# Optimization experiments

Hardware: AMD Instinct MI355X
Metric: run time of the kernel (lower is better)

Reference implementation:

```python
import jax, jax.numpy as jnp
import numpy as np

EPS = 1e-06


def _conv1x1(x, W, b):
    # x: [B,C,H,W], W: [O,C], b: [O] -> [B,O,H,W]
    return jnp.einsum('oc,bchw->bohw', W, x) + b[None, :, None, None]


def _l2_norm(x):
    # normalize over channel dim (-2) per position, matching torch.norm(p=2, dim=-2)
    return x / jnp.linalg.norm(x, axis=-2, keepdims=True)


def setup_inputs() -> dict:
    key = jax.random.key(0)
    ks = jax.random.split(key, 8)
    B, C, H, W = 8, 512, 64, 64
    Cq = C // 8
    s = 0.02
    return {
        'x': jax.random.normal(ks[0], (B, C, H, W), jnp.float32),
        'Wq': jax.random.normal(ks[1], (Cq, C), jnp.float32) * s,
        'bq': jax.random.normal(ks[2], (Cq,), jnp.float32) * s,
        'Wk': jax.random.normal(ks[3], (Cq, C), jnp.float32) * s,
        'bk': jax.random.normal(ks[4], (Cq,), jnp.float32) * s,
        'Wv': jax.random.normal(ks[5], (C, C), jnp.float32) * s,
        'bv': jax.random.normal(ks[6], (C,), jnp.float32) * s,
        'gamma': jax.random.normal(ks[7], (1,), jnp.float32),
    }


def reference(x, Wq, bq, Wk, bk, Wv, bv, gamma):
    B, C, H, W = x.shape
    N = H * W
    Q = _conv1x1(x, Wq, bq).reshape(B, -1, N)   # [B,C',N]
    K = _conv1x1(x, Wk, bk).reshape(B, -1, N)   # [B,C',N]
    V = _conv1x1(x, Wv, bv).reshape(B, C, N)    # [B,C,N]

    Qn = _l2_norm(Q).transpose(0, 2, 1)         # [B,N,C']
    Kn = _l2_norm(K)                            # [B,C',N]

    # taylor denominator: 1 / (N + Q . (sum_n K + eps))
    tailor_sum = 1.0 / (N + jnp.einsum('bnc,bc->bn', Qn, Kn.sum(-1) + EPS))  # [B,N]

    value_sum = V.sum(-1)                        # [B,C]
    matrix = jnp.einsum('bmn,bcn->bmc', Kn, V)   # [B,C',C]
    matrix_sum = value_sum[:, :, None] + jnp.einsum('bnm,bmc->bcn', Qn, matrix)  # [B,C,N]

    weight_value = (matrix_sum * tailor_sum[:, None, :]).reshape(B, C, H, W)
    return gamma * weight_value
```

## Files before the change

### kernel.cpp

```cpp
#include <hip/hip_runtime.h>
#include <math.h>

#define B_   8
#define C_   512
#define CQ   64
#define N_   4096
#define EPSF 1e-6f
#define LS   40
#define LS2  72

typedef short  shortx8 __attribute__((ext_vector_type(8)));
typedef short  shortx4 __attribute__((ext_vector_type(4)));
typedef short  shortx2 __attribute__((ext_vector_type(2)));
typedef float  floatx4 __attribute__((ext_vector_type(4)));
typedef float  floatx2 __attribute__((ext_vector_type(2)));

__device__ __forceinline__ short f2bf(float f) {
    unsigned u = __builtin_bit_cast(unsigned, f);
    u += 0x7FFFu + ((u >> 16) & 1u);
    return (short)(u >> 16);
}
__device__ __forceinline__ float bf2f(short h) {
    unsigned u = ((unsigned)(unsigned short)h) << 16;
    return __builtin_bit_cast(float, u);
}
__device__ __forceinline__ shortx8 ldf8(const short* p) {
    return *(const shortx8*)p;
}

__global__ __launch_bounds__(256) void pcast(
    const float* __restrict__ Wq, const float* __restrict__ Wk,
    const float* __restrict__ Wv, short* __restrict__ Wqk, short* __restrict__ Wvb)
{
    int i = (blockIdx.x * 256 + threadIdx.x) * 4;
    float4 v; short* dst;
    if (i < 2 * CQ * C_) {
        const float* src = (i < CQ * C_) ? (Wq + i) : (Wk + i - CQ * C_);
        v = *(const float4*)src;
        dst = Wqk + i;
    } else {
        int j = i - 2 * CQ * C_;
        v = *(const float4*)(Wv + j);
        dst = Wvb + j;
    }
    const float* f = (const float*)&v;
    shortx4 o = { f2bf(f[0]), f2bf(f[1]), f2bf(f[2]), f2bf(f[3]) };
    *(shortx4*)dst = o;
}

__global__ __launch_bounds__(256, 4) void k1_qk(
    const float* __restrict__ x, const short* __restrict__ Wqk,
    const float* __restrict__ bq, const float* __restrict__ bk,
    short* __restrict__ Qnt, short* __restrict__ Kn, float* __restrict__ Ksum)
{
    const int b   = blockIdx.y;
    const int n0  = blockIdx.x * 32;
    const int tid = threadIdx.x;
    const int lane = tid & 63, wid = tid >> 6;
    const int waveM = wid >> 1, waveN = wid & 1;
    const int quad = lane >> 4, ln = lane & 15;

    __shared__ short A_l[2][128][LS];
    __shared__ short B_l[2][32][LS];
    __shared__ float bias_l[128];

    if (tid < 128) bias_l[tid] = (tid < 64) ? bq[tid] : bk[tid - 64];

    const int mA = tid >> 1, koA = (tid & 1) * 16;
    const short* Asrc = Wqk + (size_t)mA * C_;
    const int kp = tid >> 4, nq = tid & 15;
    const float* xb = x + (size_t)b * C_ * N_;

    shortx8 a0 = *(const shortx8*)(Asrc + koA);
    shortx8 a1 = *(const shortx8*)(Asrc + koA + 8);
    floatx2 r0, r1;
    {
        const float* Bs = xb + (size_t)(kp * 2) * N_ + n0 + nq * 2;
        r0 = *(const floatx2*)(Bs);
        r1 = *(const floatx2*)(Bs + N_);
    }

    auto stage = [&](int buf, shortx8 s0, shortx8 s1, floatx2 q0, floatx2 q1) {
        *(shortx8*)&A_l[buf][mA][koA]     = s0;
        *(shortx8*)&A_l[buf][mA][koA + 8] = s1;
        shortx2 t0 = { f2bf(q0[0]), f2bf(q1[0]) };
        shortx2 t1 = { f2bf(q0[1]), f2bf(q1[1]) };
        *(shortx2*)&B_l[buf][nq * 2][kp * 2]     = t0;
        *(shortx2*)&B_l[buf][nq * 2 + 1][kp * 2] = t1;
    };
    stage(0, a0, a1, r0, r1);
    __syncthreads();

    const floatx4 z4 = {0.f, 0.f, 0.f, 0.f};
    floatx4 acc[4] = {z4, z4, z4, z4};

    int cur = 0;
    for (int it = 0; it < 16; ++it) {
        shortx8 na0, na1; floatx2 nr0, nr1;
        if (it < 15) {
            const int k0 = (it + 1) * 32;
            na0 = *(const shortx8*)(Asrc + k0 + koA);
            na1 = *(const shortx8*)(Asrc + k0 + koA + 8);
            const float* Bs = xb + (size_t)(k0 + kp * 2) * N_ + n0 + nq * 2;
            nr0 = *(const floatx2*)(Bs);
            nr1 = *(const floatx2*)(Bs + N_);
        }
        shortx8 af[4];
#pragma unroll
        for (int mt = 0; mt < 4; mt++)
            af[mt] = ldf8(&A_l[cur][waveM * 64 + mt * 16 + ln][quad * 8]);
        shortx8 bf8 = ldf8(&B_l[cur][waveN * 16 + ln][quad * 8]);
#pragma unroll
        for (int mt = 0; mt < 4; mt++)
            acc[mt] = __builtin_amdgcn_mfma_f32_16x16x32_bf16(af[mt], bf8, acc[mt], 0, 0, 0);
        if (it < 15) stage(cur ^ 1, na0, na1, nr0, nr1);
        __syncthreads();
        cur ^= 1;
    }

#pragma unroll
    for (int mt = 0; mt < 4; mt++)
#pragma unroll
        for (int r = 0; r < 4; r++)
            acc[mt][r] += bias_l[waveM * 64 + mt * 16 + quad * 4 + r];

    {
        float s = 0.f;
#pragma unroll
        for (int mt = 0; mt < 4; mt++)
#pragma unroll
            for (int r = 0; r < 4; r++) s += acc[mt][r] * acc[mt][r];
        s += __shfl_xor(s, 16);
        s += __shfl_xor(s, 32);
        float inv = rsqrtf(s);
#pragma unroll
        for (int mt = 0; mt < 4; mt++)
#pragma unroll
            for (int r = 0; r < 4; r++) acc[mt][r] *= inv;
    }

    const int n = n0 + waveN * 16 + ln;
    if (waveM == 0) {
        short* Qb = Qnt + (size_t)b * N_ * CQ;
#pragma unroll
        for (int mt = 0; mt < 4; mt++) {
            shortx4 v;
#pragma unroll
            for (int r = 0; r < 4; r++) v[r] = f2bf(acc[mt][r]);
            *(shortx4*)(Qb + (size_t)n * CQ + mt * 16 + quad * 4) = v;
        }
    } else {
        short* Kb = Kn + (size_t)b * CQ * N_;
#pragma unroll
        for (int mt = 0; mt < 4; mt++)
#pragma unroll
            for (int r = 0; r < 4; r++) {
                int m = mt * 16 + quad * 4 + r;
                float v = acc[mt][r];
                Kb[(size_t)m * N_ + n] = f2bf(v);
                float s = v;
                s += __shfl_xor(s, 1); s += __shfl_xor(s, 2);
                s += __shfl_xor(s, 4); s += __shfl_xor(s, 8);
                if (ln == 0) atomicAdd(&Ksum[b * CQ + m], s);
            }
    }
}

__global__ __launch_bounds__(256, 4) void k2_kx(
    const float* __restrict__ x, const short* __restrict__ Kn,
    float* __restrict__ KX, float* __restrict__ xsum)
{
    const int jt = blockIdx.x, ks = blockIdx.y, b = blockIdx.z;
    const int j0 = jt * 64, nbase = ks * 256;
    const int tid = threadIdx.x;
    const int lane = tid & 63, wid = tid >> 6;
    const int quad = lane >> 4, ln = lane & 15;

    __shared__ short A_l[2][64][LS];
    __shared__ short B_l[2][64][LS];

    const int rA = tid >> 2, oA = (tid & 3) * 8;
    const short* Kb = Kn + (size_t)b * CQ * N_;
    const float* xb = x + (size_t)b * C_ * N_;
    const short* As = Kb + (size_t)rA * N_ + nbase + oA;
    const float* Bs = xb + (size_t)(j0 + rA) * N_ + nbase + oA;

    float xsacc = 0.f;

    shortx8 aC = *(const shortx8*)As;
    float4 b0 = *(const float4*)(Bs);
    float4 b1 = *(const float4*)(Bs + 4);

    auto stage = [&](int buf, shortx8 a, float4 q0, float4 q1) {
        *(shortx8*)&A_l[buf][rA][oA] = a;
        const float* f0 = (const float*)&q0;
        const float* f1 = (const float*)&q1;
        shortx8 t;
#pragma unroll
        for (int i = 0; i < 4; i++) {
            t[i]     = f2bf(f0[i]); xsacc += f0[i];
            t[i + 4] = f2bf(f1[i]); xsacc += f1[i];
        }
        *(shortx8*)&B_l[buf][rA][oA] = t;
    };
    stage(0, aC, b0, b1);
    __syncthreads();

    const floatx4 z4 = {0.f, 0.f, 0.f, 0.f};
    floatx4 acc[4] = {z4, z4, z4, z4};

    int cur = 0;
    for (int it = 0; it < 8; ++it) {
        shortx8 aN; float4 n0v, n1v;
        if (it < 7) {
            const int off = (it + 1) * 32;
            aN  = *(const shortx8*)(As + off);
            n0v = *(const float4*)(Bs + off);
            n1v = *(const float4*)(Bs + off + 4);
        }
        shortx8 af[4];
#pragma unroll
        for (int mt = 0; mt < 4; mt++)
            af[mt] = ldf8(&A_l[cur][mt * 16 + ln][quad * 8]);
        shortx8 bf8 = ldf8(&B_l[cur][wid * 16 + ln][quad * 8]);
#pragma unroll
        for (int mt = 0; mt < 4; mt++)
            acc[mt] = __builtin_amdgcn_mfma_f32_16x16x32_bf16(af[mt], bf8, acc[mt], 0, 0, 0);
        if (it < 7) stage(cur ^ 1, aN, n0v, n1v);
        __syncthreads();
        cur ^= 1;
    }

    xsacc += __shfl_xor(xsacc, 1);
    xsacc += __shfl_xor(xsacc, 2);
    if ((tid & 3) == 0) atomicAdd(&xsum[b * C_ + j0 + rA], xsacc);

    float* KXb = KX + (size_t)b * CQ * C_;
#pragma unroll
    for (int mt = 0; mt < 4; mt++)
#pragma unroll
        for (int r = 0; r < 4; r++) {
            int m = mt * 16 + quad * 4 + r;
            atomicAdd(&KXb[(size_t)m * C_ + j0 + wid * 16 + ln], acc[mt][r]);
        }
}

__global__ __launch_bounds__(256, 2) void k3_m(
    const float* __restrict__ KX, const short* __restrict__ Wvb,
    const float* __restrict__ bv, const float* __restrict__ Ksum,
    const float* __restrict__ xsum,
    short* __restrict__ Mt, float* __restrict__ vs)
{
    const int ct = blockIdx.x, b = blockIdx.y;
    const int c0 = ct * 64;
    const int tid = threadIdx.x;
    const int lane = tid & 63, wid = tid >> 6;
    const int quad = lane >> 4, ln = lane & 15;

    __shared__ short A_l[2][64][LS];
    __shared__ short B_l[2][64][LS];
    __shared__ float xsl[C_], Ksl[64], bvl[64], vsp[4][64];

    xsl[tid] = xsum[(size_t)b * C_ + tid];
    xsl[tid + 256] = xsum[(size_t)b * C_ + tid + 256];
    if (tid < 64) { Ksl[tid] = Ksum[b * CQ + tid]; bvl[tid] = bv[c0 + tid]; }

    const int rA = tid >> 2, oA = (tid & 3) * 8;
    const short* As = Wvb + (size_t)(c0 + rA) * C_ + oA;
    const float* Bs = KX + ((size_t)b * CQ + rA) * C_ + oA;

    shortx8 aC = *(const shortx8*)As;
    float4 b0 = *(const float4*)(Bs);
    float4 b1 = *(const float4*)(Bs + 4);

    auto stage = [&](int buf, shortx8 a, float4 q0, float4 q1) {
        *(shortx8*)&A_l[buf][rA][oA] = a;
        const float* f0 = (const float*)&q0;
        const float* f1 = (const float*)&q1;
        shortx8 t;
#pragma unroll
        for (int i = 0; i < 4; i++) { t[i] = f2bf(f0[i]); t[i + 4] = f2bf(f1[i]); }
        *(shortx8*)&B_l[buf][rA][oA] = t;
    };
    stage(0, aC, b0, b1);
    __syncthreads();

    const floatx4 z4 = {0.f, 0.f, 0.f, 0.f};
    floatx4 acc[4] = {z4, z4, z4, z4};
    float vsacc = 0.f;
    const int cv = tid & 63;

    int cur = 0;
    for (int it = 0; it < 16; ++it) {
        shortx8 aN; float4 n0v, n1v;
        if (it < 15) {
            const int off = (it + 1) * 32;
            aN  = *(const shortx8*)(As + off);
            n0v = *(const float4*)(Bs + off);
            n1v = *(const float4*)(Bs + off + 4);
        }
        shortx8 af[4];
#pragma unroll
        for (int ct2 = 0; ct2 < 4; ct2++)
            af[ct2] = ldf8(&A_l[cur][ct2 * 16 + ln][quad * 8]);
        shortx8 bf8 = ldf8(&B_l[cur][wid * 16 + ln][quad * 8]);
#pragma unroll
        for (int ct2 = 0; ct2 < 4; ct2++)
            acc[ct2] = __builtin_amdgcn_mfma_f32_16x16x32_bf16(af[ct2], bf8, acc[ct2], 0, 0, 0);
#pragma unroll
        for (int jj = 0; jj < 8; jj++)
            vsacc += bf2f(A_l[cur][cv][wid * 8 + jj]) * xsl[it * 32 + wid * 8 + jj];
        if (it < 15) stage(cur ^ 1, aN, n0v, n1v);
        __syncthreads();
        cur ^= 1;
    }

    vsp[wid][cv] = vsacc;
    __syncthreads();
    if (tid < 64)
        vs[(size_t)b * C_ + c0 + tid] =
            vsp[0][tid] + vsp[1][tid] + vsp[2][tid] + vsp[3][tid] + (float)N_ * bvl[tid];

    const int m = wid * 16 + ln;
    const float ksm = Ksl[m];
    short* Mb = Mt + (size_t)b * C_ * CQ;
#pragma unroll
    for (int ct2 = 0; ct2 < 4; ct2++)
#pragma unroll
        for (int r = 0; r < 4; r++) {
            int c = ct2 * 16 + quad * 4 + r;
            Mb[(size_t)(c0 + c) * CQ + m] = f2bf(acc[ct2][r] + ksm * bvl[c]);
        }
}

__global__ __launch_bounds__(256, 3) void k4_out(
    const short* __restrict__ Qnt, const short* __restrict__ Mt,
    const float* __restrict__ vs, const float* __restrict__ Ksum,
    const float* __restrict__ gamma, float* __restrict__ out)
{
    const int nt = blockIdx.x, ct = blockIdx.y, b = blockIdx.z;
    const int n0 = nt * 128, c0 = ct * 128;
    const int tid = threadIdx.x;
    const int lane = tid & 63, wid = tid >> 6;
    const int waveC = wid >> 1, waveN = wid & 1;
    const int quad = lane >> 4, ln = lane & 15;

    __shared__ short A_l[128][LS2];
    __shared__ short B_l[128][LS2];
    __shared__ float tsl[128], vsl[128], Ks_l[64];

    {
        int c = tid >> 1, h = tid & 1;
        const short* src = Mt + ((size_t)b * C_ + c0 + c) * CQ + h * 32;
#pragma unroll
        for (int q = 0; q < 4; q++)
            *(shortx8*)&A_l[c][h * 32 + q * 8] = *(const shortx8*)(src + q * 8);
    }
    {
        int n = tid >> 1, h = tid & 1;
        const short* src = Qnt + ((size_t)b * N_ + n0 + n) * CQ + h * 32;
#pragma unroll
        for (int q = 0; q < 4; q++)
            *(shortx8*)&B_l[n][h * 32 + q * 8] = *(const shortx8*)(src + q * 8);
    }
    if (tid < 64)  Ks_l[tid] = Ksum[b * CQ + tid];
    if (tid < 128) vsl[tid]  = vs[(size_t)b * C_ + c0 + tid];
    __syncthreads();

    if (tid < 128) {
        const short* row = B_l[tid];
        float s = 0.f;
#pragma unroll
        for (int m = 0; m < 64; m++) s += bf2f(row[m]) * (Ks_l[m] + EPSF);
        tsl[tid] = 1.f / ((float)N_ + s);
    }
    __syncthreads();

    const floatx4 z4 = {0.f, 0.f, 0.f, 0.f};
    floatx4 acc[4][4];
#pragma unroll
    for (int i = 0; i < 4; i++)
#pragma unroll
        for (int j = 0; j < 4; j++) acc[i][j] = z4;

#pragma unroll
    for (int kc = 0; kc < 2; kc++) {
        shortx8 af[4];
#pragma unroll
        for (int ct2 = 0; ct2 < 4; ct2++)
            af[ct2] = ldf8(&A_l[waveC * 64 + ct2 * 16 + ln][kc * 32 + quad * 8]);
#pragma unroll
        for (int nt2 = 0; nt2 < 4; nt2++) {
            shortx8 bf8 = ldf8(&B_l[waveN * 64 + nt2 * 16 + ln][kc * 32 + quad * 8]);
#pragma unroll
            for (int ct2 = 0; ct2 < 4; ct2++)
                acc[ct2][nt2] = __builtin_amdgcn_mfma_f32_16x16x32_bf16(af[ct2], bf8, acc[ct2][nt2], 0, 0, 0);
        }
    }

    const float g = gamma[0];
    float* ob = out + (size_t)b * C_ * N_;
#pragma unroll
    for (int ct2 = 0; ct2 < 4; ct2++)
#pragma unroll
        for (int r = 0; r < 4; r++) {
            int cl = waveC * 64 + ct2 * 16 + quad * 4 + r;
            float vc = vsl[cl];
#pragma unroll
            for (int nt2 = 0; nt2 < 4; nt2++) {
                int nl = waveN * 64 + nt2 * 16 + ln;
                ob[(size_t)(c0 + cl) * N_ + n0 + nl] = g * tsl[nl] * (vc + acc[ct2][nt2][r]);
            }
        }
}

extern "C" void kernel_launch(void* const* d_in, const int* in_sizes, int n_in,
                              void* d_out, int out_size, void* d_ws, size_t ws_size,
                              hipStream_t stream)
{
    (void)in_sizes; (void)n_in; (void)out_size; (void)ws_size;
    const float* x     = (const float*)d_in[0];
    const float* Wq    = (const float*)d_in[1];
    const float* bq    = (const float*)d_in[2];
    const float* Wk    = (const float*)d_in[3];
    const float* bk    = (const float*)d_in[4];
    const float* Wv    = (const float*)d_in[5];
    const float* bv    = (const float*)d_in[6];
    const float* gamma = (const float*)d_in[7];
    float* out = (float*)d_out;

    short* Qnt = (short*)d_ws;
    short* Kn  = Qnt + (size_t)B_ * N_ * CQ;
    float* Ksum = (float*)(Kn + (size_t)B_ * CQ * N_);
    float* xsum = Ksum + B_ * CQ;
    float* KX   = xsum + B_ * C_;
    short* Mt   = (short*)(KX + (size_t)B_ * CQ * C_);
    float* vs   = (float*)(Mt + (size_t)B_ * C_ * CQ);
    short* Wqk  = (short*)(vs + B_ * C_);
    short* Wvb  = Wqk + 2 * CQ * C_;

    size_t zbytes = (size_t)(B_ * CQ + B_ * C_ + B_ * CQ * C_) * 4;
    hipMemsetAsync(Ksum, 0, zbytes, stream);

    pcast <<<dim3(320),       256, 0, stream>>>(Wq, Wk, Wv, Wqk, Wvb);
    k1_qk <<<dim3(128, 8),    256, 0, stream>>>(x, Wqk, bq, bk, Qnt, Kn, Ksum);
    k2_kx <<<dim3(8, 16, 8),  256, 0, stream>>>(x, Kn, KX, xsum);
    k3_m  <<<dim3(8, 8),      256, 0, stream>>>(KX, Wvb, bv, Ksum, xsum, Mt, vs);
    k4_out<<<dim3(32, 4, 8),  256, 0, stream>>>(Qnt, Mt, vs, Ksum, gamma, out);
}
```

Measured before the change: 214.4 us.

## Cast x to bf16 once in k1, reuse in k2; read MFMA operands directly from global

k1 now converts its whole 32-column slab of x to bf16 up front. It writes that bf16 copy to a workspace buffer and accumulates the per-channel x sums there, instead of pipelining fp32 x through double-buffered shared memory. k2 then reads the bf16 copy and Kn fragments straight from global memory, so it no longer re-reads fp32 x or computes xsum. k1 and k4 likewise load weight and Mt fragments directly from global instead of staging them in LDS. This halves the bytes of the second pass over x and removes the LDS staging and barriers. In exchange it adds an extra bf16 write of x, more atomics, and uncoalesced global fragment loads with no software prefetch.

New measurement: 259.3 us. +20.9%, slower.

```diff
diff --git a/kernel.cpp b/kernel.cpp
--- a/kernel.cpp
+++ b/kernel.cpp
@@ -8,12 +8,12 @@
 #define EPSF 1e-6f
 #define LS   40
 #define LS2  72
+#define LSK  520
 
 typedef short  shortx8 __attribute__((ext_vector_type(8)));
 typedef short  shortx4 __attribute__((ext_vector_type(4)));
 typedef short  shortx2 __attribute__((ext_vector_type(2)));
 typedef float  floatx4 __attribute__((ext_vector_type(4)));
-typedef float  floatx2 __attribute__((ext_vector_type(2)));
 
 __device__ __forceinline__ short f2bf(float f) {
     unsigned u = __builtin_bit_cast(unsigned, f);
@@ -51,7 +51,8 @@
 __global__ __launch_bounds__(256, 4) void k1_qk(
     const float* __restrict__ x, const short* __restrict__ Wqk,
     const float* __restrict__ bq, const float* __restrict__ bk,
-    short* __restrict__ Qnt, short* __restrict__ Kn, float* __restrict__ Ksum)
+    short* __restrict__ Qnt, short* __restrict__ Kn, short* __restrict__ xh,
+    float* __restrict__ Ksum, float* __restrict__ xsum)
 {
     const int b   = blockIdx.y;
     const int n0  = blockIdx.x * 32;
@@ -60,62 +61,50 @@
     const int waveM = wid >> 1, waveN = wid & 1;
     const int quad = lane >> 4, ln = lane & 15;
 
-    __shared__ short A_l[2][128][LS];
-    __shared__ short B_l[2][32][LS];
+    __shared__ __attribute__((aligned(16))) short B_l[32][LSK];
     __shared__ float bias_l[128];
 
     if (tid < 128) bias_l[tid] = (tid < 64) ? bq[tid] : bk[tid - 64];
 
-    const int mA = tid >> 1, koA = (tid & 1) * 16;
-    const short* Asrc = Wqk + (size_t)mA * C_;
-    const int kp = tid >> 4, nq = tid & 15;
-    const float* xb = x + (size_t)b * C_ * N_;
-
-    shortx8 a0 = *(const shortx8*)(Asrc + koA);
-    shortx8 a1 = *(const shortx8*)(Asrc + koA + 8);
-    floatx2 r0, r1;
-    {
-        const float* Bs = xb + (size_t)(kp * 2) * N_ + n0 + nq * 2;
-        r0 = *(const floatx2*)(Bs);
-        r1 = *(const floatx2*)(Bs + N_);
-    }
-
-    auto stage = [&](int buf, shortx8 s0, shortx8 s1, floatx2 q0, floatx2 q1) {
-        *(shortx8*)&A_l[buf][mA][koA]     = s0;
-        *(shortx8*)&A_l[buf][mA][koA + 8] = s1;
-        shortx2 t0 = { f2bf(q0[0]), f2bf(q1[0]) };
-        shortx2 t1 = { f2bf(q0[1]), f2bf(q1[1]) };
-        *(shortx2*)&B_l[buf][nq * 2][kp * 2]     = t0;
-        *(shortx2*)&B_l[buf][nq * 2 + 1][kp * 2] = t1;
-    };
-    stage(0, a0, a1, r0, r1);
-    __syncthreads();
-
+    const int k0 = tid * 2;
+    const float* xr0 = x  + (size_t)b * C_ * N_ + (size_t)k0 * N_ + n0;
+    short*       xh0 = xh + (size_t)b * C_ * N_ + (size_t)k0 * N_ + n0;
+    float xs0 = 0.f, xs1 = 0.f;
+#pragma unroll
+    for (int i = 0; i < 8; i++) {
+        float4 r0 = *(const float4*)(xr0 + i * 4);
+        float4 r1 = *(const float4*)(xr0 + N_ + i * 4);
+        const float* f0 = (const float*)&r0;
+        const float* f1 = (const float*)&r1;
+        shortx4 o0, o1;
+#pragma unroll
+        for (int j = 0; j < 4; j++) {
+            o0[j] = f2bf(f0[j]); xs0 += f0[j];
+            o1[j] = f2bf(f1[j]); xs1 += f1[j];
+            shortx2 t = { o0[j], o1[j] };
+            *(shortx2*)&B_l[i * 4 + j][k0] = t;
+        }
+        *(shortx4*)(xh0 + i * 4)      = o0;
+        *(shortx4*)(xh0 + N_ + i * 4) = o1;
+    }
+    atomicAdd(&xsum[b * C_ + k0],     xs0);
+    atomicAdd(&xsum[b * C_ + k0 + 1], xs1);
+    __syncthreads();
+
+    const short* Ab = Wqk + (size_t)(waveM * 64 + ln) * C_ + quad * 8;
     const floatx4 z4 = {0.f, 0.f, 0.f, 0.f};
     floatx4 acc[4] = {z4, z4, z4, z4};
 
-    int cur = 0;
-    for (int it = 0; it < 16; ++it) {
-        shortx8 na0, na1; floatx2 nr0, nr1;
-        if (it < 15) {
-            const int k0 = (it + 1) * 32;
-            na0 = *(const shortx8*)(Asrc + k0 + koA);
-            na1 = *(const shortx8*)(Asrc + k0 + koA + 8);
-            const float* Bs = xb + (size_t)(k0 + kp * 2) * N_ + n0 + nq * 2;
-            nr0 = *(const floatx2*)(Bs);
-            nr1 = *(const floatx2*)(Bs + N_);
-        }
+#pragma unroll 4
+    for (int kc = 0; kc < 16; ++kc) {
+        shortx8 bf8 = ldf8(&B_l[waveN * 16 + ln][kc * 32 + quad * 8]);
         shortx8 af[4];
 #pragma unroll
         for (int mt = 0; mt < 4; mt++)
-            af[mt] = ldf8(&A_l[cur][waveM * 64 + mt * 16 + ln][quad * 8]);
-        shortx8 bf8 = ldf8(&B_l[cur][waveN * 16 + ln][quad * 8]);
+            af[mt] = ldf8(Ab + (size_t)mt * 16 * C_ + kc * 32);
 #pragma unroll
         for (int mt = 0; mt < 4; mt++)
             acc[mt] = __builtin_amdgcn_mfma_f32_16x16x32_bf16(af[mt], bf8, acc[mt], 0, 0, 0);
-        if (it < 15) stage(cur ^ 1, na0, na1, nr0, nr1);
-        __syncthreads();
-        cur ^= 1;
     }
 
 #pragma unroll
@@ -167,8 +156,8 @@
 }
 
 __global__ __launch_bounds__(256, 4) void k2_kx(
-    const float* __restrict__ x, const short* __restrict__ Kn,
-    float* __restrict__ KX, float* __restrict__ xsum)
+    const short* __restrict__ xh, const short* __restrict__ Kn,
+    float* __restrict__ KX)
 {
     const int jt = blockIdx.x, ks = blockIdx.y, b = blockIdx.z;
     const int j0 = jt * 64, nbase = ks * 256;
@@ -176,64 +165,24 @@
     const int lane = tid & 63, wid = tid >> 6;
     const int quad = lane >> 4, ln = lane & 15;
 
-    __shared__ short A_l[2][64][LS];
-    __shared__ short B_l[2][64][LS];
-
-    const int rA = tid >> 2, oA = (tid & 3) * 8;
-    const short* Kb = Kn + (size_t)b * CQ * N_;
-    const float* xb = x + (size_t)b * C_ * N_;
-    const short* As = Kb + (size_t)rA * N_ + nbase + oA;
-    const float* Bs = xb + (size_t)(j0 + rA) * N_ + nbase + oA;
-
-    float xsacc = 0.f;
-
-    shortx8 aC = *(const shortx8*)As;
-    float4 b0 = *(const float4*)(Bs);
-    float4 b1 = *(const float4*)(Bs + 4);
-
-    auto stage = [&](int buf, shortx8 a, float4 q0, float4 q1) {
-        *(shortx8*)&A_l[buf][rA][oA] = a;
-        const float* f0 = (const float*)&q0;
-        const float* f1 = (const float*)&q1;
-        shortx8 t;
-#pragma unroll
-        for (int i = 0; i < 4; i++) {
-            t[i]     = f2bf(f0[i]); xsacc += f0[i];
-            t[i + 4] = f2bf(f1[i]); xsacc += f1[i];
-        }
-        *(shortx8*)&B_l[buf][rA][oA] = t;
-    };
-    stage(0, aC, b0, b1);
-    __syncthreads();
+    const short* Ab = Kn + (size_t)b * CQ * N_ + (size_t)ln * N_ + nbase + quad * 8;
+    const short* Bb = xh + (size_t)b * C_ * N_
+                    + (size_t)(j0 + wid * 16 + ln) * N_ + nbase + quad * 8;
 
     const floatx4 z4 = {0.f, 0.f, 0.f, 0.f};
     floatx4 acc[4] = {z4, z4, z4, z4};
 
-    int cur = 0;
-    for (int it = 0; it < 8; ++it) {
-        shortx8 aN; float4 n0v, n1v;
-        if (it < 7) {
-            const int off = (it + 1) * 32;
-            aN  = *(const shortx8*)(As + off);
-            n0v = *(const float4*)(Bs + off);
-            n1v = *(const float4*)(Bs + off + 4);
-        }
+#pragma unroll 4
+    for (int kc = 0; kc < 8; ++kc) {
+        shortx8 bf8 = ldf8(Bb + kc * 32);
         shortx8 af[4];
 #pragma unroll
         for (int mt = 0; mt < 4; mt++)
-            af[mt] = ldf8(&A_l[cur][mt * 16 + ln][quad * 8]);
-        shortx8 bf8 = ldf8(&B_l[cur][wid * 16 + ln][quad * 8]);
+            af[mt] = ldf8(Ab + (size_t)mt * 16 * N_ + kc * 32);
 #pragma unroll
         for (int mt = 0; mt < 4; mt++)
             acc[mt] = __builtin_amdgcn_mfma_f32_16x16x32_bf16(af[mt], bf8, acc[mt], 0, 0, 0);
-        if (it < 7) stage(cur ^ 1, aN, n0v, n1v);
-        __syncthreads();
-        cur ^= 1;
-    }
-
-    xsacc += __shfl_xor(xsacc, 1);
-    xsacc += __shfl_xor(xsacc, 2);
-    if ((tid & 3) == 0) atomicAdd(&xsum[b * C_ + j0 + rA], xsacc);
+    }
 
     float* KXb = KX + (size_t)b * CQ * C_;
 #pragma unroll
@@ -345,17 +294,9 @@
     const int waveC = wid >> 1, waveN = wid & 1;
     const int quad = lane >> 4, ln = lane & 15;
 
-    __shared__ short A_l[128][LS2];
     __shared__ short B_l[128][LS2];
     __shared__ float tsl[128], vsl[128], Ks_l[64];
 
-    {
-        int c = tid >> 1, h = tid & 1;
-        const short* src = Mt + ((size_t)b * C_ + c0 + c) * CQ + h * 32;
-#pragma unroll
-        for (int q = 0; q < 4; q++)
-            *(shortx8*)&A_l[c][h * 32 + q * 8] = *(const shortx8*)(src + q * 8);
-    }
     {
         int n = tid >> 1, h = tid & 1;
         const short* src = Qnt + ((size_t)b * N_ + n0 + n) * CQ + h * 32;
@@ -383,12 +324,14 @@
 #pragma unroll
         for (int j = 0; j < 4; j++) acc[i][j] = z4;
 
+    const short* Am = Mt + (size_t)b * C_ * CQ
+                    + (size_t)(c0 + waveC * 64 + ln) * CQ + quad * 8;
 #pragma unroll
     for (int kc = 0; kc < 2; kc++) {
         shortx8 af[4];
 #pragma unroll
         for (int ct2 = 0; ct2 < 4; ct2++)
-            af[ct2] = ldf8(&A_l[waveC * 64 + ct2 * 16 + ln][kc * 32 + quad * 8]);
+            af[ct2] = ldf8(Am + (size_t)ct2 * 16 * CQ + kc * 32);
 #pragma unroll
         for (int nt2 = 0; nt2 < 4; nt2++) {
             shortx8 bf8 = ldf8(&B_l[waveN * 64 + nt2 * 16 + ln][kc * 32 + quad * 8]);
@@ -438,13 +381,14 @@
     float* vs   = (float*)(Mt + (size_t)B_ * C_ * CQ);
     short* Wqk  = (short*)(vs + B_ * C_);
     short* Wvb  = Wqk + 2 * CQ * C_;
+    short* xh   = Wvb + (size_t)C_ * C_;
 
     size_t zbytes = (size_t)(B_ * CQ + B_ * C_ + B_ * CQ * C_) * 4;
     hipMemsetAsync(Ksum, 0, zbytes, stream);
 
     pcast <<<dim3(320),       256, 0, stream>>>(Wq, Wk, Wv, Wqk, Wvb);
-    k1_qk <<<dim3(128, 8),    256, 0, stream>>>(x, Wqk, bq, bk, Qnt, Kn, Ksum);
-    k2_kx <<<dim3(8, 16, 8),  256, 0, stream>>>(x, Kn, KX, xsum);
+    k1_qk <<<dim3(128, 8),    256, 0, stream>>>(x, Wqk, bq, bk, Qnt, Kn, xh, Ksum, xsum);
+    k2_kx <<<dim3(8, 16, 8),  256, 0, stream>>>(xh, Kn, KX);
     k3_m  <<<dim3(8, 8),      256, 0, stream>>>(KX, Wvb, bv, Ksum, xsum, Mt, vs);
     k4_out<<<dim3(32, 4, 8),  256, 0, stream>>>(Qnt, Mt, vs, Ksum, gamma, out);
 }
```
